# Kernel optimization log

Measured on AMD Instinct MI355X. Metric: run time of the kernel, lower is better.

The kernel has to match this reference:

```python
import jax, jax.numpy as jnp
import numpy as np

jax.config.update("jax_enable_x64", True)  # original uses double for Cholesky stability

LAM = 1.0


def _safe_pow(x, a):
    # |x|**a, with a gradient-safe handling of x == 0 (result is 0 for a > 0;
    # naive 0**a has nan grad w.r.t. a via log(0)).
    ax = jnp.abs(x)
    safe = jnp.where(ax == 0, 1.0, ax)
    return jnp.where(ax == 0, 0.0, safe ** a)


def _dx_cov(alpha, tau, T):
    # fGn (increment) covariance; stationary -> depends only on lag k = j - i (Toeplitz)
    t = jnp.arange(T - 1, dtype=jnp.float64)
    DT = (t[None, :] - t[:, None])[None, :, :]          # [1, T-1, T-1]
    a = alpha[:, None, None].astype(jnp.float64)        # [BS, 1, 1]
    tb = tau[:, None, None].astype(jnp.float64)
    R = 0.5 * (_safe_pow(DT + 1.0, a) + _safe_pow(DT - 1.0, a) - 2.0 * _safe_pow(DT, a))
    adt = jnp.abs(DT)
    # exponential taper beyond lag tau; clamp exponent so unused branch can't overflow
    decay = jnp.exp(-LAM * jnp.maximum(adt - tb, 0.0))
    R = jnp.where(adt >= tb, R * decay, R)
    return R                                            # [BS, T-1, T-1] float64


def setup_inputs() -> dict:
    key = jax.random.key(0)
    k1, k2, k3, k4 = jax.random.split(key, 4)
    BS, T, dim = 64, 1024, 3
    alpha = (0.5 + jax.random.uniform(k1, (BS,))).astype(jnp.float32)        # (0.5, 1.5) valid fBM exponent
    tau = (20.0 + 50.0 * jax.random.uniform(k2, (BS,))).astype(jnp.float32)  # taper lag > 0
    diffusion = (0.5 + jax.random.uniform(k3, (BS,))).astype(jnp.float32)
    du = jax.random.normal(k4, (BS, T - 1, dim), dtype=jnp.float32)          # hoisted torch.randn
    return {"alpha": alpha, "tau": tau, "diffusion": diffusion, "du": du, "T": T}


def reference(alpha, tau, diffusion, du, T):
    BS, dim = alpha.shape[0], du.shape[-1]
    C = _dx_cov(alpha, tau, T)                           # [BS, T-1, T-1] float64
    L = jnp.linalg.cholesky(C).astype(jnp.float32)       # batched Cholesky, cast like torch
    du_s = du * jnp.sqrt(diffusion)[:, None, None]       # scale noise by sqrt(D)
    dx = L @ du_s                                        # [BS, T-1, dim]
    x = jnp.cumsum(dx, axis=1)
    zeros = jnp.zeros((BS, 1, dim), dtype=x.dtype)
    return jnp.concatenate([zeros, x], axis=1)           # [BS, T, dim]
```

## Files before the change

### kernel.cpp

```cpp
#include <hip/hip_runtime.h>
#include <math.h>


#define TM1 1023
#define NTH 256
#define K0  128

__device__ __forceinline__ float bperm(int a, float v) {
    return __int_as_float(__builtin_amdgcn_ds_bpermute(a, __float_as_int(v)));
}
__device__ __forceinline__ float rdlane(float v, int s) {
    return __int_as_float(__builtin_amdgcn_readlane(__float_as_int(v), s));
}
__device__ __forceinline__ int uslot(int k) { return ((k & 3) << 8) | (k >> 2); }

__global__ __launch_bounds__(NTH, 1)
void fbm_schur_kernel(const float* __restrict__ alpha,
                      const float* __restrict__ tau,
                      const float* __restrict__ diffusion,
                      const float* __restrict__ du,
                      float* __restrict__ out)
{
    const int b   = blockIdx.x;
    const int tid = threadIdx.x;
    const int w   = tid >> 6;
    const int l   = tid & 63;

    __shared__ float  colD[K0 * 128];
    __shared__ float4 us4[1024];
    __shared__ float  yx[1024], yy[1024], yz[1024];
    __shared__ float  Lc[128];
    __shared__ float  wtot[12];

    const float sd = sqrtf(diffusion[b]);
    const float* dub = du + (size_t)b * (TM1 * 3);

    for (int e = tid; e < TM1 * 3; e += NTH) {
        int k = e / 3, d = e - 3 * k;
        ((float*)&us4[uslot(k)])[d] = dub[e] * sd;
    }
    for (int i = tid; i < 1024; i += NTH) { yx[i] = 0.f; yy[i] = 0.f; yz[i] = 0.f; }

    float g1a = 0.f, g1b = 0.f, g2a = 0.f, g2b = 0.f;
    if (w == 0) {
        const double a  = (double)alpha[b];
        const double tb = (double)tau[b];
        auto cov = [&](int k) -> float {
            if (k == 0) return 1.0f;
            double dk = (double)k;
            double ck = 0.5 * (pow(dk + 1.0, a) + pow(dk - 1.0, a) - 2.0 * pow(dk, a));
            if (dk >= tb) ck *= exp(tb - dk);
            return (float)ck;
        };
        g1a = cov(l);
        g1b = cov(l + 64);
        g2a = (l == 0) ? 0.f : g1a;
        g2b = g1b;
    }
    __syncthreads();

    if (w == 0) {
        const int addr_up = ((l + 1) & 63) << 2;
        for (int k = 0; k < K0; ++k) {
            colD[k * 128 + l]      = g1a;
            colD[k * 128 + 64 + l] = g1b;
            float den  = rdlane(g1a, 0);
            float num  = rdlane(g2a, 1);
            float r    = num * __builtin_amdgcn_rcpf(den);
            float wrap = rdlane(g2b, 0);
            float g2pa = bperm(addr_up, g2a);
            float g2pb = bperm(addr_up, g2b);
            if (l == 63) { g2pa = wrap; g2pb = 0.f; }
            float n1a = fmaf(-r, g2pa, g1a);
            float n1b = fmaf(-r, g2pb, g1b);
            g2a = fmaf(-r, g1a, g2pa);
            g2b = fmaf(-r, g1b, g2pb);
            g1a = n1a; g1b = n1b;
        }
        float sc = __frsqrt_rn(rdlane(g1a, 0));
        Lc[l]      = g1a * sc;
        Lc[64 + l] = g1b * sc;
    }
    __syncthreads();

    {
        float4 v0 = us4[uslot(l)];
        float4 v1 = us4[uslot(64 + l)];
        float i0 = __frsqrt_rn(colD[l * 128]);
        float i1 = __frsqrt_rn(colD[(64 + l) * 128]);
        float ucx0 = v0.x * i0, ucy0 = v0.y * i0, ucz0 = v0.z * i0;
        float ucx1 = v1.x * i1, ucy1 = v1.y * i1, ucz1 = v1.z * i1;

        float ax = 0.f, ay = 0.f, az = 0.f;
        #pragma unroll 4
        for (int k2 = 0; k2 < 64; ++k2) {
            int p = tid - k2;
            float v = colD[k2 * 128 + p];
            v = ((unsigned)p < 128u) ? v : 0.f;
            ax = fmaf(v, rdlane(ucx0, k2), ax);
            ay = fmaf(v, rdlane(ucy0, k2), ay);
            az = fmaf(v, rdlane(ucz0, k2), az);
        }
        #pragma unroll 4
        for (int k2 = 64; k2 < 128; ++k2) {
            int p = tid - k2;
            float v = colD[k2 * 128 + p];
            v = ((unsigned)p < 128u) ? v : 0.f;
            ax = fmaf(v, rdlane(ucx1, k2 - 64), ax);
            ay = fmaf(v, rdlane(ucy1, k2 - 64), ay);
            az = fmaf(v, rdlane(ucz1, k2 - 64), az);
        }
        yx[tid] = ax; yy[tid] = ay; yz[tid] = az;
    }
    __syncthreads();

    {
        float lca = Lc[l], lcb = Lc[64 + l];
        const int B = K0 + 4 * tid;
        float4 q0 = us4[uslot(B + 0)];
        float4 q1 = us4[uslot(B + 1)];
        float4 q2 = us4[uslot(B + 2)];
        float4 q3 = us4[uslot(B + 3)];
        float a0x=0,a0y=0,a0z=0, a1x=0,a1y=0,a1z=0;
        float a2x=0,a2y=0,a2z=0, a3x=0,a3y=0,a3z=0;

        #pragma unroll 8
        for (int j = 0; j < 64; ++j) {
            float lc = rdlane(lca, j);
            a0x = fmaf(lc, q0.x, a0x); a0y = fmaf(lc, q0.y, a0y); a0z = fmaf(lc, q0.z, a0z);
            a1x = fmaf(lc, q1.x, a1x); a1y = fmaf(lc, q1.y, a1y); a1z = fmaf(lc, q1.z, a1z);
            a2x = fmaf(lc, q2.x, a2x); a2y = fmaf(lc, q2.y, a2y); a2z = fmaf(lc, q2.z, a2z);
            a3x = fmaf(lc, q3.x, a3x); a3y = fmaf(lc, q3.y, a3y); a3z = fmaf(lc, q3.z, a3z);
            int xi = B - j - 1;
            float4 nv = us4[uslot(xi)];
            bool ok = (xi >= K0);
            nv.x = ok ? nv.x : 0.f; nv.y = ok ? nv.y : 0.f; nv.z = ok ? nv.z : 0.f;
            q3 = q2; q2 = q1; q1 = q0; q0 = nv;
        }
        #pragma unroll 8
        for (int j = 64; j < 128; ++j) {
            float lc = rdlane(lcb, j - 64);
            a0x = fmaf(lc, q0.x, a0x); a0y = fmaf(lc, q0.y, a0y); a0z = fmaf(lc, q0.z, a0z);
            a1x = fmaf(lc, q1.x, a1x); a1y = fmaf(lc, q1.y, a1y); a1z = fmaf(lc, q1.z, a1z);
            a2x = fmaf(lc, q2.x, a2x); a2y = fmaf(lc, q2.y, a2y); a2z = fmaf(lc, q2.z, a2z);
            a3x = fmaf(lc, q3.x, a3x); a3y = fmaf(lc, q3.y, a3y); a3z = fmaf(lc, q3.z, a3z);
            int xi = B - j - 1;
            float4 nv = us4[uslot(xi)];
            bool ok = (xi >= K0);
            nv.x = ok ? nv.x : 0.f; nv.y = ok ? nv.y : 0.f; nv.z = ok ? nv.z : 0.f;
            q3 = q2; q2 = q1; q1 = q0; q0 = nv;
        }
        if (B + 0 <= 1022) { yx[B+0] += a0x; yy[B+0] += a0y; yz[B+0] += a0z; }
        if (B + 1 <= 1022) { yx[B+1] += a1x; yy[B+1] += a1y; yz[B+1] += a1z; }
        if (B + 2 <= 1022) { yx[B+2] += a2x; yy[B+2] += a2y; yz[B+2] += a2z; }
        if (B + 3 <= 1022) { yx[B+3] += a3x; yy[B+3] += a3y; yz[B+3] += a3z; }
    }
    __syncthreads();

    float cx = 0.f, cy = 0.f, cz = 0.f;
    for (int s = 0; s < 4; ++s) {
        int i = (w << 8) + (s << 6) + l;
        float sx = (i < TM1) ? yx[i] : 0.f;
        float sy = (i < TM1) ? yy[i] : 0.f;
        float sz = (i < TM1) ? yz[i] : 0.f;
        #pragma unroll
        for (int off = 1; off < 64; off <<= 1) {
            float tx = __shfl_up(sx, off);
            float ty = __shfl_up(sy, off);
            float tz = __shfl_up(sz, off);
            if (l >= off) { sx += tx; sy += ty; sz += tz; }
        }
        sx += cx; sy += cy; sz += cz;
        if (i < TM1) { yx[i] = sx; yy[i] = sy; yz[i] = sz; }
        cx = __shfl(sx, 63); cy = __shfl(sy, 63); cz = __shfl(sz, 63);
    }
    if (l == 0) { wtot[w * 3 + 0] = cx; wtot[w * 3 + 1] = cy; wtot[w * 3 + 2] = cz; }
    __syncthreads();

    float ox = 0.f, oy = 0.f, oz = 0.f;
    for (int q = 0; q < w; ++q) {
        ox += wtot[q * 3 + 0]; oy += wtot[q * 3 + 1]; oz += wtot[q * 3 + 2];
    }
    float* outb = out + (size_t)b * (TM1 + 1) * 3;
    for (int s = 0; s < 4; ++s) {
        int i = (w << 8) + (s << 6) + l;
        if (i < TM1) {
            outb[(i + 1) * 3 + 0] = yx[i] + ox;
            outb[(i + 1) * 3 + 1] = yy[i] + oy;
            outb[(i + 1) * 3 + 2] = yz[i] + oz;
        }
    }
    if (tid == 0) { outb[0] = 0.f; outb[1] = 0.f; outb[2] = 0.f; }
}

extern "C" void kernel_launch(void* const* d_in, const int* in_sizes, int n_in,
                              void* d_out, int out_size, void* d_ws, size_t ws_size,
                              hipStream_t stream)
{
    const float* alpha     = (const float*)d_in[0];
    const float* tau       = (const float*)d_in[1];
    const float* diffusion = (const float*)d_in[2];
    const float* du        = (const float*)d_in[3];
    float* out = (float*)d_out;
    const int BS = in_sizes[0];

    fbm_schur_kernel<<<dim3(BS), dim3(NTH), 0, stream>>>(
        alpha, tau, diffusion, du, out);
}
```

Before: 86.51 us.

## Quadruple threads, split convolution by lag quarters, overlap noise load with Schur

The block grows from 256 to 1024 threads. The banded convolution is split so each wave handles a quarter of the 128 lags for 256 output rows, and partial sums are reduced through shared memory. Loading and scaling the noise now runs on the other waves while wave 0 runs the Schur recursion, which writes normalized L columns transposed (padded stride) so the head rows merge into one pass. It also swaps ds_bpermute for a DPP row shift, guarded by a runtime probe, and simplifies the scan to one element per thread. The risks are more register pressure at 1024 threads, and the serial Schur loop on one wave stays the critical path.

```diff
diff --git a/kernel.cpp b/kernel.cpp
--- a/kernel.cpp
+++ b/kernel.cpp
@@ -3,8 +3,9 @@
 
 
 #define TM1 1023
-#define NTH 256
+#define NTH 1024
 #define K0  128
+#define CSTRIDE 129
 
 __device__ __forceinline__ float bperm(int a, float v) {
     return __int_as_float(__builtin_amdgcn_ds_bpermute(a, __float_as_int(v)));
@@ -12,7 +13,60 @@
 __device__ __forceinline__ float rdlane(float v, int s) {
     return __int_as_float(__builtin_amdgcn_readlane(__float_as_int(v), s));
 }
+__device__ __forceinline__ float dpp_shl1(float v) {
+    return __int_as_float(__builtin_amdgcn_update_dpp(
+        0, __float_as_int(v), 0x130, 0xF, 0xF, true));
+}
 __device__ __forceinline__ int uslot(int k) { return ((k & 3) << 8) | (k >> 2); }
+
+__device__ __forceinline__ float4 ldus(const float4* us4s, int k) {
+    int kc = (k < 0) ? 0 : k;
+    float4 v = us4s[uslot(kc)];
+    if (k < 0) { v.x = 0.f; v.y = 0.f; v.z = 0.f; }
+    return v;
+}
+
+template<bool MIXED>
+__device__ __forceinline__ void conv_quad(
+    const float4* us4s, const float* colDT, float lca, float lcb,
+    int B, int jq, int quad, float4* ypx4, float4* ypy4, float4* ypz4)
+{
+    const int   j0   = jq << 5;
+    const float lsel = (jq < 2) ? lca : lcb;
+
+    float4 q0 = MIXED ? ldus(us4s, B + 0 - j0) : us4s[uslot(B + 0 - j0)];
+    float4 q1 = MIXED ? ldus(us4s, B + 1 - j0) : us4s[uslot(B + 1 - j0)];
+    float4 q2 = MIXED ? ldus(us4s, B + 2 - j0) : us4s[uslot(B + 2 - j0)];
+    float4 q3 = MIXED ? ldus(us4s, B + 3 - j0) : us4s[uslot(B + 3 - j0)];
+
+    float a0x=0,a0y=0,a0z=0, a1x=0,a1y=0,a1z=0;
+    float a2x=0,a2y=0,a2z=0, a3x=0,a3y=0,a3z=0;
+
+    #pragma unroll 8
+    for (int jj = 0; jj < 32; ++jj) {
+        const int j = j0 + jj;
+        float lcj = rdlane(lsel, j & 63);
+        float c0 = lcj, c1 = lcj, c2 = lcj, c3 = lcj;
+        if (MIXED) {
+            int p = B - j;
+            float4 h = *reinterpret_cast<const float4*>(&colDT[(j << 7) + B]);
+            c0 = (p + 0 < 128) ? h.x : lcj;
+            c1 = (p + 1 < 128) ? h.y : lcj;
+            c2 = (p + 2 < 128) ? h.z : lcj;
+            c3 = (p + 3 < 128) ? h.w : lcj;
+        }
+        a0x = fmaf(c0, q0.x, a0x); a0y = fmaf(c0, q0.y, a0y); a0z = fmaf(c0, q0.z, a0z);
+        a1x = fmaf(c1, q1.x, a1x); a1y = fmaf(c1, q1.y, a1y); a1z = fmaf(c1, q1.z, a1z);
+        a2x = fmaf(c2, q2.x, a2x); a2y = fmaf(c2, q2.y, a2y); a2z = fmaf(c2, q2.z, a2z);
+        a3x = fmaf(c3, q3.x, a3x); a3y = fmaf(c3, q3.y, a3y); a3z = fmaf(c3, q3.z, a3z);
+        int xi = B - j - 1;
+        float4 nv = MIXED ? ldus(us4s, xi) : us4s[uslot(xi)];
+        q3 = q2; q2 = q1; q1 = q0; q0 = nv;
+    }
+    ypx4[(jq << 8) + quad] = make_float4(a0x, a1x, a2x, a3x);
+    ypy4[(jq << 8) + quad] = make_float4(a0y, a1y, a2y, a3y);
+    ypz4[(jq << 8) + quad] = make_float4(a0z, a1z, a2z, a3z);
+}
 
 __global__ __launch_bounds__(NTH, 1)
 void fbm_schur_kernel(const float* __restrict__ alpha,
@@ -26,23 +80,26 @@
     const int w   = tid >> 6;
     const int l   = tid & 63;
 
-    __shared__ float  colD[K0 * 128];
+    __shared__ float  colDT[K0 * CSTRIDE];
     __shared__ float4 us4[1024];
-    __shared__ float  yx[1024], yy[1024], yz[1024];
+    __shared__ float4 ypx4[4 * 256];
+    __shared__ float4 ypy4[4 * 256];
+    __shared__ float4 ypz4[4 * 256];
     __shared__ float  Lc[128];
-    __shared__ float  wtot[12];
+    __shared__ float  wtot[48];
 
     const float sd = sqrtf(diffusion[b]);
     const float* dub = du + (size_t)b * (TM1 * 3);
 
-    for (int e = tid; e < TM1 * 3; e += NTH) {
-        int k = e / 3, d = e - 3 * k;
-        ((float*)&us4[uslot(k)])[d] = dub[e] * sd;
-    }
-    for (int i = tid; i < 1024; i += NTH) { yx[i] = 0.f; yy[i] = 0.f; yz[i] = 0.f; }
-
-    float g1a = 0.f, g1b = 0.f, g2a = 0.f, g2b = 0.f;
-    if (w == 0) {
+    if (w > 0) {
+        for (int e = tid - 64; e < TM1 * 3; e += (NTH - 64)) {
+            int k = e / 3, d = e - 3 * k;
+            ((float*)&us4[uslot(k)])[d] = dub[e] * sd;
+        }
+        for (int i = tid - 64; i < K0; i += (NTH - 64))
+            colDT[i * CSTRIDE + 128] = 0.f;
+        if (tid == 64) us4[uslot(1023)] = make_float4(0.f, 0.f, 0.f, 0.f);
+    } else {
         const double a  = (double)alpha[b];
         const double tb = (double)tau[b];
         auto cov = [&](int k) -> float {
@@ -52,31 +109,39 @@
             if (dk >= tb) ck *= exp(tb - dk);
             return (float)ck;
         };
-        g1a = cov(l);
-        g1b = cov(l + 64);
-        g2a = (l == 0) ? 0.f : g1a;
-        g2b = g1b;
-    }
-    __syncthreads();
-
-    if (w == 0) {
+        float g1a = cov(l);
+        float g1b = cov(l + 64);
+        float g2a = (l == 0) ? 0.f : g1a;
+        float g2b = g1b;
+
+        int probe = __builtin_amdgcn_update_dpp(0, l + 100, 0x130, 0xF, 0xF, true);
+        const bool dpp_ok = (__builtin_amdgcn_readlane(probe, 5) == 106);
         const int addr_up = ((l + 1) & 63) << 2;
-        for (int k = 0; k < K0; ++k) {
-            colD[k * 128 + l]      = g1a;
-            colD[k * 128 + 64 + l] = g1b;
-            float den  = rdlane(g1a, 0);
-            float num  = rdlane(g2a, 1);
-            float r    = num * __builtin_amdgcn_rcpf(den);
-            float wrap = rdlane(g2b, 0);
-            float g2pa = bperm(addr_up, g2a);
-            float g2pb = bperm(addr_up, g2b);
-            if (l == 63) { g2pa = wrap; g2pb = 0.f; }
-            float n1a = fmaf(-r, g2pa, g1a);
-            float n1b = fmaf(-r, g2pb, g1b);
-            g2a = fmaf(-r, g1a, g2pa);
-            g2b = fmaf(-r, g1b, g2pb);
-            g1a = n1a; g1b = n1b;
-        }
+
+#define SCHUR_LOOP(SHA, SHB)                                               \
+        for (int k = 0; k < K0; ++k) {                                     \
+            float den  = rdlane(g1a, 0);                                   \
+            float sc   = __frsqrt_rn(den);                                 \
+            colDT[l * CSTRIDE + k]        = g1a * sc;                      \
+            colDT[(64 + l) * CSTRIDE + k] = g1b * sc;                      \
+            float num  = rdlane(g2a, 1);                                   \
+            float r    = num * __builtin_amdgcn_rcpf(den);                 \
+            float wrap = rdlane(g2b, 0);                                   \
+            float g2pa = (SHA);                                            \
+            float g2pb = (SHB);                                            \
+            if (l == 63) { g2pa = wrap; g2pb = 0.f; }                      \
+            float n1a = fmaf(-r, g2pa, g1a);                               \
+            float n1b = fmaf(-r, g2pb, g1b);                               \
+            g2a = fmaf(-r, g1a, g2pa);                                     \
+            g2b = fmaf(-r, g1b, g2pb);                                     \
+            g1a = n1a; g1b = n1b;                                          \
+        }
+        if (dpp_ok) {
+            SCHUR_LOOP(dpp_shl1(g2a), dpp_shl1(g2b))
+        } else {
+            SCHUR_LOOP(bperm(addr_up, g2a), bperm(addr_up, g2b))
+        }
+#undef SCHUR_LOOP
         float sc = __frsqrt_rn(rdlane(g1a, 0));
         Lc[l]      = g1a * sc;
         Lc[64 + l] = g1b * sc;
@@ -84,97 +149,36 @@
     __syncthreads();
 
     {
-        float4 v0 = us4[uslot(l)];
-        float4 v1 = us4[uslot(64 + l)];
-        float i0 = __frsqrt_rn(colD[l * 128]);
-        float i1 = __frsqrt_rn(colD[(64 + l) * 128]);
-        float ucx0 = v0.x * i0, ucy0 = v0.y * i0, ucz0 = v0.z * i0;
-        float ucx1 = v1.x * i1, ucy1 = v1.y * i1, ucz1 = v1.z * i1;
-
-        float ax = 0.f, ay = 0.f, az = 0.f;
-        #pragma unroll 4
-        for (int k2 = 0; k2 < 64; ++k2) {
-            int p = tid - k2;
-            float v = colD[k2 * 128 + p];
-            v = ((unsigned)p < 128u) ? v : 0.f;
-            ax = fmaf(v, rdlane(ucx0, k2), ax);
-            ay = fmaf(v, rdlane(ucy0, k2), ay);
-            az = fmaf(v, rdlane(ucz0, k2), az);
-        }
-        #pragma unroll 4
-        for (int k2 = 64; k2 < 128; ++k2) {
-            int p = tid - k2;
-            float v = colD[k2 * 128 + p];
-            v = ((unsigned)p < 128u) ? v : 0.f;
-            ax = fmaf(v, rdlane(ucx1, k2 - 64), ax);
-            ay = fmaf(v, rdlane(ucy1, k2 - 64), ay);
-            az = fmaf(v, rdlane(ucz1, k2 - 64), az);
-        }
-        yx[tid] = ax; yy[tid] = ay; yz[tid] = az;
+        float lca = Lc[l], lcb = Lc[64 + l];
+        const int jq   = w & 3;
+        const int rb   = w >> 2;
+        const int quad = (rb << 6) + l;
+        const int B    = quad << 2;
+        if (rb == 0)
+            conv_quad<true >(us4, colDT, lca, lcb, B, jq, quad, ypx4, ypy4, ypz4);
+        else
+            conv_quad<false>(us4, colDT, lca, lcb, B, jq, quad, ypx4, ypy4, ypz4);
     }
     __syncthreads();
 
-    {
-        float lca = Lc[l], lcb = Lc[64 + l];
-        const int B = K0 + 4 * tid;
-        float4 q0 = us4[uslot(B + 0)];
-        float4 q1 = us4[uslot(B + 1)];
-        float4 q2 = us4[uslot(B + 2)];
-        float4 q3 = us4[uslot(B + 3)];
-        float a0x=0,a0y=0,a0z=0, a1x=0,a1y=0,a1z=0;
-        float a2x=0,a2y=0,a2z=0, a3x=0,a3y=0,a3z=0;
-
-        #pragma unroll 8
-        for (int j = 0; j < 64; ++j) {
-            float lc = rdlane(lca, j);
-            a0x = fmaf(lc, q0.x, a0x); a0y = fmaf(lc, q0.y, a0y); a0z = fmaf(lc, q0.z, a0z);
-            a1x = fmaf(lc, q1.x, a1x); a1y = fmaf(lc, q1.y, a1y); a1z = fmaf(lc, q1.z, a1z);
-            a2x = fmaf(lc, q2.x, a2x); a2y = fmaf(lc, q2.y, a2y); a2z = fmaf(lc, q2.z, a2z);
-            a3x = fmaf(lc, q3.x, a3x); a3y = fmaf(lc, q3.y, a3y); a3z = fmaf(lc, q3.z, a3z);
-            int xi = B - j - 1;
-            float4 nv = us4[uslot(xi)];
-            bool ok = (xi >= K0);
-            nv.x = ok ? nv.x : 0.f; nv.y = ok ? nv.y : 0.f; nv.z = ok ? nv.z : 0.f;
-            q3 = q2; q2 = q1; q1 = q0; q0 = nv;
-        }
-        #pragma unroll 8
-        for (int j = 64; j < 128; ++j) {
-            float lc = rdlane(lcb, j - 64);
-            a0x = fmaf(lc, q0.x, a0x); a0y = fmaf(lc, q0.y, a0y); a0z = fmaf(lc, q0.z, a0z);
-            a1x = fmaf(lc, q1.x, a1x); a1y = fmaf(lc, q1.y, a1y); a1z = fmaf(lc, q1.z, a1z);
-            a2x = fmaf(lc, q2.x, a2x); a2y = fmaf(lc, q2.y, a2y); a2z = fmaf(lc, q2.z, a2z);
-            a3x = fmaf(lc, q3.x, a3x); a3y = fmaf(lc, q3.y, a3y); a3z = fmaf(lc, q3.z, a3z);
-            int xi = B - j - 1;
-            float4 nv = us4[uslot(xi)];
-            bool ok = (xi >= K0);
-            nv.x = ok ? nv.x : 0.f; nv.y = ok ? nv.y : 0.f; nv.z = ok ? nv.z : 0.f;
-            q3 = q2; q2 = q1; q1 = q0; q0 = nv;
-        }
-        if (B + 0 <= 1022) { yx[B+0] += a0x; yy[B+0] += a0y; yz[B+0] += a0z; }
-        if (B + 1 <= 1022) { yx[B+1] += a1x; yy[B+1] += a1y; yz[B+1] += a1z; }
-        if (B + 2 <= 1022) { yx[B+2] += a2x; yy[B+2] += a2y; yz[B+2] += a2z; }
-        if (B + 3 <= 1022) { yx[B+3] += a3x; yy[B+3] += a3y; yz[B+3] += a3z; }
-    }
-    __syncthreads();
-
-    float cx = 0.f, cy = 0.f, cz = 0.f;
-    for (int s = 0; s < 4; ++s) {
-        int i = (w << 8) + (s << 6) + l;
-        float sx = (i < TM1) ? yx[i] : 0.f;
-        float sy = (i < TM1) ? yy[i] : 0.f;
-        float sz = (i < TM1) ? yz[i] : 0.f;
-        #pragma unroll
-        for (int off = 1; off < 64; off <<= 1) {
-            float tx = __shfl_up(sx, off);
-            float ty = __shfl_up(sy, off);
-            float tz = __shfl_up(sz, off);
-            if (l >= off) { sx += tx; sy += ty; sz += tz; }
-        }
-        sx += cx; sy += cy; sz += cz;
-        if (i < TM1) { yx[i] = sx; yy[i] = sy; yz[i] = sz; }
-        cx = __shfl(sx, 63); cy = __shfl(sy, 63); cz = __shfl(sz, 63);
-    }
-    if (l == 0) { wtot[w * 3 + 0] = cx; wtot[w * 3 + 1] = cy; wtot[w * 3 + 2] = cz; }
+    const int i = tid;
+    float sx = 0.f, sy = 0.f, sz = 0.f;
+    if (i < TM1) {
+        const float* px = (const float*)ypx4;
+        const float* py = (const float*)ypy4;
+        const float* pz = (const float*)ypz4;
+        sx = px[i] + px[1024 + i] + px[2048 + i] + px[3072 + i];
+        sy = py[i] + py[1024 + i] + py[2048 + i] + py[3072 + i];
+        sz = pz[i] + pz[1024 + i] + pz[2048 + i] + pz[3072 + i];
+    }
+    #pragma unroll
+    for (int off = 1; off < 64; off <<= 1) {
+        float tx = __shfl_up(sx, off);
+        float ty = __shfl_up(sy, off);
+        float tz = __shfl_up(sz, off);
+        if (l >= off) { sx += tx; sy += ty; sz += tz; }
+    }
+    if (l == 63) { wtot[w * 3 + 0] = sx; wtot[w * 3 + 1] = sy; wtot[w * 3 + 2] = sz; }
     __syncthreads();
 
     float ox = 0.f, oy = 0.f, oz = 0.f;
@@ -182,13 +186,10 @@
         ox += wtot[q * 3 + 0]; oy += wtot[q * 3 + 1]; oz += wtot[q * 3 + 2];
     }
     float* outb = out + (size_t)b * (TM1 + 1) * 3;
-    for (int s = 0; s < 4; ++s) {
-        int i = (w << 8) + (s << 6) + l;
-        if (i < TM1) {
-            outb[(i + 1) * 3 + 0] = yx[i] + ox;
-            outb[(i + 1) * 3 + 1] = yy[i] + oy;
-            outb[(i + 1) * 3 + 2] = yz[i] + oz;
-        }
+    if (i < TM1) {
+        outb[(i + 1) * 3 + 0] = sx + ox;
+        outb[(i + 1) * 3 + 1] = sy + oy;
+        outb[(i + 1) * 3 + 2] = sz + oz;
     }
     if (tid == 0) { outb[0] = 0.f; outb[1] = 0.f; outb[2] = 0.f; }
 }
```

New measurement: 76.50 us. 11.6% less time.
